# Kernel optimization log

Measured on AMD Instinct MI355X. Metric: run time of the kernel, lower is better.

Reference implementation:

```python
import jax, jax.numpy as jnp
import numpy as np

HEADS = 8
DH = 64      # dim_head
KS = 3       # kernel_size (padding=1, stride=1, dilation=1 -> same-resolution window)


def _unfold3x3(t):
    # t: [b, c, H, W] -> patches [b, c, 9, H, W], window positions in row-major
    # order, matching torch F.unfold channel ordering (c major, kernel pos minor).
    b, c, H, W = t.shape
    tp = jnp.pad(t, ((0, 0), (0, 0), (1, 1), (1, 1)))
    return jnp.stack([tp[:, :, i:i + H, j:j + W]
                      for i in range(KS) for j in range(KS)], axis=2)


def setup_inputs() -> dict:
    key = jax.random.key(0)
    k0, k1, k2, k3 = jax.random.split(key, 4)
    b, c, H, W = 16, 256, 32, 32
    inner = HEADS * DH  # 512
    x = jax.random.normal(k0, (b, c, H, W), jnp.float32)
    Wq = jax.random.normal(k1, (inner, c), jnp.float32) * 0.02      # to_q 1x1 conv
    Wkv = jax.random.normal(k2, (2 * inner, c), jnp.float32) * 0.02  # to_kv 1x1 conv (k=1)
    Wo = jax.random.normal(k3, (c, inner), jnp.float32) * 0.02       # to_out 1x1 conv
    bo = jnp.zeros((c,), jnp.float32)
    return {"x": x, "Wq": Wq, "Wkv": Wkv, "Wo": Wo, "bo": bo}


def reference(x, Wq, Wkv, Wo, bo):
    b, c, H, W = x.shape
    n = H * W
    w = KS * KS
    scale = DH ** -0.5

    # 1x1 convs as channel matmuls
    q = jnp.einsum('bcxy,oc->boxy', x, Wq)               # [b, h*d, H, W]
    q = q.reshape(b, HEADS, DH, n).transpose(0, 1, 3, 2)  # [b, h, n, d]
    kv = jnp.einsum('bcxy,oc->boxy', x, Wkv)
    k, v = jnp.split(kv, 2, axis=1)                       # each [b, h*d, H, W]

    def to_windows(t):
        p = _unfold3x3(t)                                  # [b, h*d, 9, H, W]
        return p.reshape(b, HEADS, DH, w, n).transpose(0, 1, 4, 3, 2)  # [b,h,n,w,d]

    k = to_windows(k)
    v = to_windows(v)

    # einsum over d directly == original repeat(q over w) + elementwise*sum
    dots = jnp.einsum('bhnd,bhnwd->bhnw', q, k) * scale
    attn = jax.nn.softmax(dots, axis=-1)
    out = jnp.einsum('bhnw,bhnwd->bhnd', attn, v)          # [b, h, n, d]
    out = out.transpose(0, 1, 3, 2).reshape(b, HEADS * DH, H, W)
    out = jnp.einsum('bcxy,oc->boxy', out, Wo) + bo[None, :, None, None]
    return (out, attn)
```

## Files before the change

kernel.cpp:

```cpp
#include <hip/hip_runtime.h>

#define NPIX   1024
#define BATCH  16
#define CIN    256
#define NQKV   1536
#define INNER  512
#define HEADS  8
#define DH     64

typedef __attribute__((ext_vector_type(8))) short short8;
typedef __attribute__((ext_vector_type(4))) float f32x4;

__device__ __forceinline__ ushort f2b(float f) {
    union { float f; unsigned u; } v; v.f = f;
    unsigned r = v.u + 0x7fffu + ((v.u >> 16) & 1u);
    return (ushort)(r >> 16);
}
__device__ __forceinline__ float b2f(ushort u) {
    union { float f; unsigned u; } v; v.u = ((unsigned)u) << 16; return v.f;
}
__device__ __forceinline__ void async16(const void* g, void* l) {
    __builtin_amdgcn_global_load_lds((const __attribute__((address_space(1))) void*)g,
                                     (__attribute__((address_space(3))) void*)l, 16, 0, 0);
}

__global__ __launch_bounds__(256) void prep_all(const float* __restrict__ x,
        const float* __restrict__ Wq, const float* __restrict__ Wkv,
        const float* __restrict__ Wo, ushort* __restrict__ xT,
        ushort* __restrict__ Wqkv_b, ushort* __restrict__ Wob) {
    const int bid = blockIdx.x;
    const int t   = threadIdx.x;
    if (bid < 1024) {
        __shared__ float tf[64][65];
        const int b   = bid >> 6;
        const int rem = bid & 63;
        const int p0  = (rem & 15) * 64;
        const int c0  = (rem >> 4) * 64;
#pragma unroll
        for (int ps = 0; ps < 4; ps++) {
            int c = (t >> 4) + ps * 16;
            int p = (t & 15) * 4;
            float4 v = *reinterpret_cast<const float4*>(&x[(b * CIN + c0 + c) * NPIX + p0 + p]);
            tf[c][p] = v.x; tf[c][p + 1] = v.y; tf[c][p + 2] = v.z; tf[c][p + 3] = v.w;
        }
        __syncthreads();
#pragma unroll
        for (int ps = 0; ps < 2; ps++) {
            int p  = (t >> 3) + ps * 32;
            int c8 = (t & 7) * 8;
            short8 r;
#pragma unroll
            for (int j = 0; j < 8; j++) r[j] = (short)f2b(tf[c8 + j][p]);
            *reinterpret_cast<short8*>(&xT[(b * NPIX + p0 + p) * CIN + c0 + c8]) = r;
        }
    } else {
        int i = (bid - 1024) * 256 + t;
        if (i < NQKV * CIN)
            Wqkv_b[i] = f2b(i < INNER * CIN ? Wq[i] : Wkv[i - INNER * CIN]);
        int j = i - NQKV * CIN;
        if (j >= 0 && j < CIN * INNER)
            Wob[j] = f2b(Wo[j]);
    }
}

__global__ __launch_bounds__(256) void gemm_qkv(const ushort* __restrict__ xT,
        const ushort* __restrict__ Wb, ushort* __restrict__ qkv) {
    __shared__ ushort As[2][128][32];
    __shared__ ushort Bs[2][128][32];
    const int bid = blockIdx.x;
    const int swz = (bid & 7) * 192 + (bid >> 3);
    const int m0  = (swz / 12) * 128;
    const int n0  = (swz % 12) * 128;
    const int t    = threadIdx.x;
    const int wave = t >> 6, lane = t & 63;
    const int wo = (wave & 1) * 64, wp = (wave >> 1) * 64;
    const int lrow = lane & 15, loct = lane >> 4;

    const int srow = t >> 2;
    const int skb  = (t & 3) * 8;
    const ushort* gA = Wb + (n0 + srow) * CIN + skb;
    const ushort* gB = xT + (m0 + srow) * CIN + skb;

    f32x4 acc[4][4];
#pragma unroll
    for (int i = 0; i < 4; i++)
#pragma unroll
        for (int j = 0; j < 4; j++) acc[i][j] = (f32x4){0.f, 0.f, 0.f, 0.f};

#define STAGE1(buf, c0)                                             \
    do {                                                            \
        async16(gA + (c0),            &As[buf][wave * 16][0]);      \
        async16(gA + 64 * CIN + (c0), &As[buf][64 + wave * 16][0]); \
        async16(gB + (c0),            &Bs[buf][wave * 16][0]);      \
        async16(gB + 64 * CIN + (c0), &Bs[buf][64 + wave * 16][0]); \
    } while (0)

    STAGE1(0, 0);
    __syncthreads();
    int cur = 0;
    const int NT = CIN / 32;
    for (int it = 0; it < NT; ++it) {
        if (it + 1 < NT) STAGE1(cur ^ 1, (it + 1) * 32);
        short8 a[4], bb[4];
#pragma unroll
        for (int i = 0; i < 4; i++)
            a[i] = *reinterpret_cast<const short8*>(&As[cur][wo + i * 16 + lrow][loct * 8]);
#pragma unroll
        for (int j = 0; j < 4; j++)
            bb[j] = *reinterpret_cast<const short8*>(&Bs[cur][wp + j * 16 + lrow][loct * 8]);
#pragma unroll
        for (int i = 0; i < 4; i++)
#pragma unroll
            for (int j = 0; j < 4; j++)
                acc[i][j] = __builtin_amdgcn_mfma_f32_16x16x32_bf16(a[i], bb[j], acc[i][j], 0, 0, 0);
        __syncthreads();
        cur ^= 1;
    }
#undef STAGE1

#pragma unroll
    for (int i = 0; i < 4; i++)
#pragma unroll
        for (int j = 0; j < 4; j++) {
            int gm = m0 + wp + j * 16 + lrow;
            int go = n0 + wo + i * 16 + loct * 4;
            ushort4 pk = make_ushort4(f2b(acc[i][j].x), f2b(acc[i][j].y),
                                      f2b(acc[i][j].z), f2b(acc[i][j].w));
            *reinterpret_cast<ushort4*>(&qkv[gm * NQKV + go]) = pk;
        }
}

__global__ __launch_bounds__(256) void attn_kernel(const ushort* __restrict__ qkv,
        ushort* __restrict__ po, float* __restrict__ attn_out) {
    const int bid = blockIdx.x;
    const int swz = (bid & 7) * 512 + (bid >> 3);
    const int m    = swz * 4 + (threadIdx.x >> 6);
    const int lane = threadIdx.x & 63;
    const int h = lane >> 3, sub = lane & 7;
    const int b = m >> 10;
    const int p = m & 1023;
    const int py = p >> 5, px = p & 31;
    const int hd8 = h * DH + sub * 8;

    short8 qv = *reinterpret_cast<const short8*>(&qkv[m * NQKV + hd8]);
    float qf[8];
#pragma unroll
    for (int j = 0; j < 8; j++) qf[j] = b2f((ushort)qv[j]);

    float dots[9];
    int   nb[9];
    bool  ok[9];
#pragma unroll
    for (int w = 0; w < 9; w++) {
        int dy = w / 3 - 1, dx = w % 3 - 1;
        int ny = py + dy, nx = px + dx;
        bool in = ((unsigned)ny < 32u) && ((unsigned)nx < 32u);
        ok[w] = in;
        int nm = b * NPIX + ny * 32 + nx;
        nb[w] = nm;
        float d = 0.f;
        if (in) {
            short8 kv8 = *reinterpret_cast<const short8*>(&qkv[nm * NQKV + 512 + hd8]);
#pragma unroll
            for (int j = 0; j < 8; j++) d = fmaf(qf[j], b2f((ushort)kv8[j]), d);
        }
        d += __shfl_xor(d, 1);
        d += __shfl_xor(d, 2);
        d += __shfl_xor(d, 4);
        dots[w] = d * 0.125f;
    }

    float mx = dots[0];
#pragma unroll
    for (int w = 1; w < 9; w++) mx = fmaxf(mx, dots[w]);
    float e[9], s = 0.f;
#pragma unroll
    for (int w = 0; w < 9; w++) { e[w] = __expf(dots[w] - mx); s += e[w]; }
    const float inv = 1.f / s;

    float o[8] = {};
#pragma unroll
    for (int w = 0; w < 9; w++) {
        if (ok[w]) {
            short8 vv = *reinterpret_cast<const short8*>(&qkv[nb[w] * NQKV + 1024 + hd8]);
            float pw = e[w] * inv;
#pragma unroll
            for (int j = 0; j < 8; j++) o[j] = fmaf(pw, b2f((ushort)vv[j]), o[j]);
        }
    }
    short8 r;
#pragma unroll
    for (int j = 0; j < 8; j++) r[j] = (short)f2b(o[j]);
    *reinterpret_cast<short8*>(&po[m * INNER + hd8]) = r;

    float* ab = &attn_out[((b * HEADS + h) * NPIX + p) * 9];
    ab[sub] = e[sub] * inv;
    if (sub == 0) ab[8] = e[8] * inv;
}

__global__ __launch_bounds__(256) void gemm_out(const ushort* __restrict__ po,
        const ushort* __restrict__ Wob, const float* __restrict__ bo,
        float* __restrict__ out) {
    __shared__ ushort As[2][128][32];
    __shared__ ushort Bs[2][128][32];
    const int m0 = blockIdx.x * 128;
    const int n0 = blockIdx.y * 128;
    const int t    = threadIdx.x;
    const int wave = t >> 6, lane = t & 63;
    const int wm = (wave >> 1) * 64, wn = (wave & 1) * 64;
    const int lrow = lane & 15, loct = lane >> 4;

    const int srow = t >> 2;
    const int skb  = (t & 3) * 8;
    const ushort* gA = po  + (m0 + srow) * INNER + skb;
    const ushort* gB = Wob + (n0 + srow) * INNER + skb;

    f32x4 acc[4][4];
#pragma unroll
    for (int i = 0; i < 4; i++)
#pragma unroll
        for (int j = 0; j < 4; j++) acc[i][j] = (f32x4){0.f, 0.f, 0.f, 0.f};

#define STAGE2(buf, c0)                                               \
    do {                                                              \
        async16(gA + (c0),              &As[buf][wave * 16][0]);      \
        async16(gA + 64 * INNER + (c0), &As[buf][64 + wave * 16][0]); \
        async16(gB + (c0),              &Bs[buf][wave * 16][0]);      \
        async16(gB + 64 * INNER + (c0), &Bs[buf][64 + wave * 16][0]); \
    } while (0)

    STAGE2(0, 0);
    __syncthreads();
    int cur = 0;
    const int NT = INNER / 32;
    for (int it = 0; it < NT; ++it) {
        if (it + 1 < NT) STAGE2(cur ^ 1, (it + 1) * 32);
        short8 a[4], bb[4];
#pragma unroll
        for (int i = 0; i < 4; i++)
            a[i] = *reinterpret_cast<const short8*>(&As[cur][wm + i * 16 + lrow][loct * 8]);
#pragma unroll
        for (int j = 0; j < 4; j++)
            bb[j] = *reinterpret_cast<const short8*>(&Bs[cur][wn + j * 16 + lrow][loct * 8]);
#pragma unroll
        for (int i = 0; i < 4; i++)
#pragma unroll
            for (int j = 0; j < 4; j++)
                acc[i][j] = __builtin_amdgcn_mfma_f32_16x16x32_bf16(a[i], bb[j], acc[i][j], 0, 0, 0);
        __syncthreads();
        cur ^= 1;
    }
#undef STAGE2

    const int bb_ = m0 >> 10;
    const int p0  = m0 & 1023;
#pragma unroll
    for (int i = 0; i < 4; i++)
#pragma unroll
        for (int j = 0; j < 4; j++) {
            int o  = n0 + wn + j * 16 + lrow;
            int pp = p0 + wm + i * 16 + loct * 4;
            float bias = bo[o];
            float4 v = make_float4(acc[i][j].x + bias, acc[i][j].y + bias,
                                   acc[i][j].z + bias, acc[i][j].w + bias);
            *reinterpret_cast<float4*>(&out[(bb_ * CIN + o) * NPIX + pp]) = v;
        }
}

extern "C" void kernel_launch(void* const* d_in, const int* in_sizes, int n_in,
                              void* d_out, int out_size, void* d_ws, size_t ws_size,
                              hipStream_t stream) {
    const float* x   = (const float*)d_in[0];
    const float* Wq  = (const float*)d_in[1];
    const float* Wkv = (const float*)d_in[2];
    const float* Wo  = (const float*)d_in[3];
    const float* bo  = (const float*)d_in[4];

    float* out  = (float*)d_out;
    float* attn = out + BATCH * CIN * NPIX;

    ushort* xT     = (ushort*)d_ws;
    ushort* Wqkv_b = xT + 16384 * CIN;
    ushort* Wob    = Wqkv_b + NQKV * CIN;
    ushort* qkv    = Wob + CIN * INNER;
    ushort* po     = qkv + 16384 * NQKV;

    prep_all<<<3072, 256, 0, stream>>>(x, Wq, Wkv, Wo, xT, Wqkv_b, Wob);

    gemm_qkv<<<1536, 256, 0, stream>>>(xT, Wqkv_b, qkv);

    attn_kernel<<<16384 / 4, 256, 0, stream>>>(qkv, po, attn);

    gemm_out<<<dim3(128, 2), 256, 0, stream>>>(po, Wob, bo, out);
}
```

Measured before the change: 139.3 us.

## Enlarge QKV GEMM tile to 256x128 with MFMA-fragment-ordered LDS layout

Doubles the M tile of the QKV projection GEMM so each wave computes a 64x128 output block, and halves the grid to match. The LDS layout is also changed so each 16-row x 32-k fragment is stored contiguously in the order a wave reads it, which removes bank conflicts on the fragment loads. This is meant to raise arithmetic intensity per LDS load and cut global traffic for the weight tile. The cost is double the accumulator registers (128 floats per lane), which could limit occupancy even with the launch bound of 2 blocks, and fewer blocks per CU.

```diff
diff --git a/kernel.cpp b/kernel.cpp
--- a/kernel.cpp
+++ b/kernel.cpp
@@ -63,36 +63,43 @@
     }
 }
 
-__global__ __launch_bounds__(256) void gemm_qkv(const ushort* __restrict__ xT,
+__global__ __launch_bounds__(256, 2) void gemm_qkv(const ushort* __restrict__ xT,
         const ushort* __restrict__ Wb, ushort* __restrict__ qkv) {
-    __shared__ ushort As[2][128][32];
-    __shared__ ushort Bs[2][128][32];
+    __shared__ ushort As[2][4096];
+    __shared__ ushort Bs[2][8192];
     const int bid = blockIdx.x;
-    const int swz = (bid & 7) * 192 + (bid >> 3);
-    const int m0  = (swz / 12) * 128;
+    const int swz = (bid & 7) * 96 + (bid >> 3);
+    const int m0  = (swz / 12) * 256;
     const int n0  = (swz % 12) * 128;
     const int t    = threadIdx.x;
     const int wave = t >> 6, lane = t & 63;
-    const int wo = (wave & 1) * 64, wp = (wave >> 1) * 64;
+    const int wo = (wave & 1) * 64;
+    const int wp = (wave >> 1) * 128;
     const int lrow = lane & 15, loct = lane >> 4;
 
-    const int srow = t >> 2;
-    const int skb  = (t & 3) * 8;
-    const ushort* gA = Wb + (n0 + srow) * CIN + skb;
-    const ushort* gB = xT + (m0 + srow) * CIN + skb;
-
-    f32x4 acc[4][4];
+    const int rlo = (lane & 15);
+    const int k8  = (lane >> 4) * 8;
+    const ushort* gA0 = Wb + (n0 + (0 * 4 + wave) * 16 + rlo) * CIN + k8;
+    const ushort* gA1 = Wb + (n0 + (1 * 4 + wave) * 16 + rlo) * CIN + k8;
+    const ushort* gB0 = xT + (m0 + (0 * 4 + wave) * 16 + rlo) * CIN + k8;
+    const ushort* gB1 = xT + (m0 + (1 * 4 + wave) * 16 + rlo) * CIN + k8;
+    const ushort* gB2 = xT + (m0 + (2 * 4 + wave) * 16 + rlo) * CIN + k8;
+    const ushort* gB3 = xT + (m0 + (3 * 4 + wave) * 16 + rlo) * CIN + k8;
+
+    f32x4 acc[4][8];
 #pragma unroll
     for (int i = 0; i < 4; i++)
 #pragma unroll
-        for (int j = 0; j < 4; j++) acc[i][j] = (f32x4){0.f, 0.f, 0.f, 0.f};
-
-#define STAGE1(buf, c0)                                             \
-    do {                                                            \
-        async16(gA + (c0),            &As[buf][wave * 16][0]);      \
-        async16(gA + 64 * CIN + (c0), &As[buf][64 + wave * 16][0]); \
-        async16(gB + (c0),            &Bs[buf][wave * 16][0]);      \
-        async16(gB + 64 * CIN + (c0), &Bs[buf][64 + wave * 16][0]); \
+        for (int j = 0; j < 8; j++) acc[i][j] = (f32x4){0.f, 0.f, 0.f, 0.f};
+
+#define STAGE1(buf, koff)                                     \
+    do {                                                      \
+        async16(gA0 + (koff), &As[buf][wave * 512]);          \
+        async16(gA1 + (koff), &As[buf][2048 + wave * 512]);   \
+        async16(gB0 + (koff), &Bs[buf][wave * 512]);          \
+        async16(gB1 + (koff), &Bs[buf][2048 + wave * 512]);   \
+        async16(gB2 + (koff), &Bs[buf][4096 + wave * 512]);   \
+        async16(gB3 + (koff), &Bs[buf][6144 + wave * 512]);   \
     } while (0)
 
     STAGE1(0, 0);
@@ -101,17 +108,21 @@
     const int NT = CIN / 32;
     for (int it = 0; it < NT; ++it) {
         if (it + 1 < NT) STAGE1(cur ^ 1, (it + 1) * 32);
-        short8 a[4], bb[4];
+        short8 a[4], bb[8];
+#pragma unroll
+        for (int i = 0; i < 4; i++) {
+            int chunk = (wave & 1) * 4 + i;
+            a[i] = *reinterpret_cast<const short8*>(&As[cur][(chunk * 64 + lane) * 8]);
+        }
+#pragma unroll
+        for (int j = 0; j < 8; j++) {
+            int chunk = (wave >> 1) * 8 + j;
+            bb[j] = *reinterpret_cast<const short8*>(&Bs[cur][(chunk * 64 + lane) * 8]);
+        }
 #pragma unroll
         for (int i = 0; i < 4; i++)
-            a[i] = *reinterpret_cast<const short8*>(&As[cur][wo + i * 16 + lrow][loct * 8]);
-#pragma unroll
-        for (int j = 0; j < 4; j++)
-            bb[j] = *reinterpret_cast<const short8*>(&Bs[cur][wp + j * 16 + lrow][loct * 8]);
-#pragma unroll
-        for (int i = 0; i < 4; i++)
-#pragma unroll
-            for (int j = 0; j < 4; j++)
+#pragma unroll
+            for (int j = 0; j < 8; j++)
                 acc[i][j] = __builtin_amdgcn_mfma_f32_16x16x32_bf16(a[i], bb[j], acc[i][j], 0, 0, 0);
         __syncthreads();
         cur ^= 1;
@@ -121,7 +132,7 @@
 #pragma unroll
     for (int i = 0; i < 4; i++)
 #pragma unroll
-        for (int j = 0; j < 4; j++) {
+        for (int j = 0; j < 8; j++) {
             int gm = m0 + wp + j * 16 + lrow;
             int go = n0 + wo + i * 16 + loct * 4;
             ushort4 pk = make_ushort4(f2b(acc[i][j].x), f2b(acc[i][j].y),
@@ -287,7 +298,7 @@
 
     prep_all<<<3072, 256, 0, stream>>>(x, Wq, Wkv, Wo, xT, Wqkv_b, Wob);
 
-    gemm_qkv<<<1536, 256, 0, stream>>>(xT, Wqkv_b, qkv);
+    gemm_qkv<<<768, 256, 0, stream>>>(xT, Wqkv_b, qkv);
 
     attn_kernel<<<16384 / 4, 256, 0, stream>>>(qkv, po, attn);
 
```

Result: slower. 147.0 us (+5.6%).
